# Kernel tuning notes

Hardware: AMD Instinct MI355X
Metric: run time of the kernel (lower is better)

## Reference

```python
import jax, jax.numpy as jnp
import numpy as np

B, S, D, H, F, V = 64, 64, 512, 8, 2048, 8192
L = 6
ENC_C = 2048  # InceptionV3 feature channels
NEG_INF = jnp.float32(-jnp.inf)


def _layernorm(x, g, b, eps=1e-3):
    mu = jnp.mean(x, axis=-1, keepdims=True)
    var = jnp.var(x, axis=-1, keepdims=True)
    return (x - mu) * jax.lax.rsqrt(var + eps) * g + b


def _mha(q_in, kv_in, Wq, Wk, Wv, Wo, causal=False):
    Bq, Sq, Dm = q_in.shape
    Sk = kv_in.shape[1]
    dh = Dm // H
    q = (q_in @ Wq).reshape(Bq, Sq, H, dh)
    k = (kv_in @ Wk).reshape(Bq, Sk, H, dh)
    v = (kv_in @ Wv).reshape(Bq, Sk, H, dh)
    scores = jnp.einsum('bqhd,bkhd->bhqk', q, k) / jnp.sqrt(jnp.float32(dh))
    if causal:
        mask = jnp.tril(jnp.ones((Sq, Sk), dtype=bool))
        scores = jnp.where(mask, scores, jnp.float32(-1e9))
    a = jax.nn.softmax(scores, axis=-1)
    o = jnp.einsum('bhqk,bkhd->bqhd', a, v).reshape(Bq, Sq, Dm)
    return o @ Wo


def replacement_mask(targets):
    # out[b,i,v] = -inf iff some j<=i has targets[b,j]==v and v!=0
    valid = (targets != 0)[..., None].astype(jnp.float32)  # (B,S,1)
    oh = jax.nn.one_hot(targets, V, dtype=jnp.float32) * valid  # (B,S,V)
    seen = jnp.cumsum(oh, axis=1) > 0
    return jnp.where(seen, NEG_INF, jnp.float32(0.0))


def setup_inputs() -> dict:
    key = jax.random.key(0)
    ks = jax.random.split(key, 32)
    n = lambda i, shp, sc=0.02: jax.random.normal(ks[i], shp, jnp.float32) * sc
    inp = {
        'enc_feat': jax.random.normal(ks[0], (B, 8, 8, ENC_C), jnp.float32),
        'targets': jax.random.randint(ks[1], (B, S), 0, V, jnp.int32),
        'conv_w': n(2, (ENC_C, D)), 'conv_b': jnp.zeros((D,), jnp.float32),
        'tok_emb': n(3, (V, D)), 'pos_emb': n(4, (S, D)),
        'Wq_s': n(5, (L, D, D)), 'Wk_s': n(6, (L, D, D)),
        'Wv_s': n(7, (L, D, D)), 'Wo_s': n(8, (L, D, D)),
        'Wq_c': n(9, (L, D, D)), 'Wk_c': n(10, (L, D, D)),
        'Wv_c': n(11, (L, D, D)), 'Wo_c': n(12, (L, D, D)),
        'W1': n(13, (L, D, F)), 'fb1': jnp.zeros((L, F), jnp.float32),
        'W2': n(14, (L, F, D)), 'fb2': jnp.zeros((L, D), jnp.float32),
        'g1': jnp.ones((L, D), jnp.float32), 'be1': jnp.zeros((L, D), jnp.float32),
        'g2': jnp.ones((L, D), jnp.float32), 'be2': jnp.zeros((L, D), jnp.float32),
        'g3': jnp.ones((L, D), jnp.float32), 'be3': jnp.zeros((L, D), jnp.float32),
        'Wout': n(15, (D, V)), 'bout': jnp.zeros((V,), jnp.float32),
    }
    return inp


def reference(enc_feat, conv_w, conv_b, tok_emb, pos_emb,
              Wq_s, Wk_s, Wv_s, Wo_s, Wq_c, Wk_c, Wv_c, Wo_c,
              W1, fb1, W2, fb2, g1, be1, g2, be2, g3, be3,
              Wout, bout, targets):
    # 1x1 conv == per-pixel matmul, then flatten spatial -> (B, 64, D)
    enc = enc_feat.reshape(B, -1, ENC_C) @ conv_w + conv_b
    # decoder: token + positional embedding
    x = tok_emb[targets] + pos_emb[None, :, :]
    for l in range(L):
        a1 = _mha(x, x, Wq_s[l], Wk_s[l], Wv_s[l], Wo_s[l], causal=True)
        x = _layernorm(x + a1, g1[l], be1[l])
        a2 = _mha(x, enc, Wq_c[l], Wk_c[l], Wv_c[l], Wo_c[l])
        x = _layernorm(x + a2, g2[l], be2[l])
        ff = jax.nn.relu(x @ W1[l] + fb1[l]) @ W2[l] + fb2[l]
        x = _layernorm(x + ff, g3[l], be3[l])
    logits = x @ Wout + bout
    return logits + replacement_mask(targets)
```

## Files before the change

kernel.cpp:

```cpp
#include <hip/hip_runtime.h>
#include <cstdint>
#include <cstddef>

#define SS   64
#define BB   64
#define DM   512
#define NH   8
#define DH   64
#define FF   2048
#define VV   8192
#define LL   6
#define ENCC 2048
#define MR   4096

#define MASK_SENTINEL -3.0e38f

typedef unsigned short u16;
typedef __attribute__((ext_vector_type(8))) short bf16x8;
typedef __attribute__((ext_vector_type(4))) float f32x4;

__device__ __forceinline__ u16 f2b(float f) {
    union { float f; uint32_t u; } c; c.f = f;
    uint32_t u = c.u;
    return (u16)((u + 0x7fffu + ((u >> 16) & 1u)) >> 16);
}
__device__ __forceinline__ float blo(uint32_t p) {
    union { uint32_t u; float f; } c; c.u = p << 16; return c.f;
}
__device__ __forceinline__ float bhi(uint32_t p) {
    union { uint32_t u; float f; } c; c.u = p & 0xffff0000u; return c.f;
}

#define GLL(g, l) __builtin_amdgcn_global_load_lds( \
    (const __attribute__((address_space(1))) void*)(g), \
    (__attribute__((address_space(3))) void*)(l), 16, 0, 0)

template<int BMT>
__global__ __launch_bounds__(256) void gemm_bf16(
    const u16* __restrict__ A, const u16* __restrict__ BT,
    const float* __restrict__ bias, u16* __restrict__ Cb,
    int K, int ldc, int relu, int nsplit,
    const u16* __restrict__ A2, const u16* __restrict__ BT2,
    u16* __restrict__ C2, int ldc2)
{
    constexpr int WM = BMT / 2;
    constexpr int AI = WM / 16;
    __shared__ __align__(16) char smem[16384];
    u16* As = (u16*)smem;
    u16* Bs = As + BMT * 32;
    const int tid = threadIdx.x;
    const int wave = tid >> 6, lane = tid & 63;

    int bx = blockIdx.x;
    const u16* Ab = A; const u16* Bb = BT; u16* Cp = Cb; int ld = ldc;
    const float* bi = bias; int rl = relu;
    if (bx >= nsplit) { bx -= nsplit; Ab = A2; Bb = BT2; Cp = C2; ld = ldc2; bi = nullptr; rl = 0; }

    const int m0 = blockIdx.y * BMT, n0 = bx * 128;
    const int srow = wave * 16 + (lane >> 2);
    const int scol = (lane & 3) * 8;
    const u16* Ap  = Ab + (size_t)(m0 + srow) * K + scol;
    const u16* Bp  = Bb + (size_t)(n0 + srow) * K + scol;
    const u16* Ap2 = Ap + (size_t)64 * K;
    const u16* Bp2 = Bp + (size_t)64 * K;
    u16* AsW = As + wave * 16 * 32;
    u16* BsW = Bs + wave * 16 * 32;

    const int wm = wave >> 1, wn = wave & 1;
    const int q = lane >> 4, mr = lane & 15;
    const u16* aRd = As + (size_t)(wm * WM + mr) * 32 + q * 8;
    const u16* bRd = Bs + (size_t)(wn * 64 + mr) * 32 + q * 8;

    f32x4 acc[AI][4];
    const f32x4 z = {0.f, 0.f, 0.f, 0.f};
#pragma unroll
    for (int i = 0; i < AI; i++)
#pragma unroll
        for (int j = 0; j < 4; j++) acc[i][j] = z;

    for (int k0 = 0; k0 < K; k0 += 32) {
        GLL(Ap, AsW);
        if constexpr (BMT == 128) GLL(Ap2, AsW + 64 * 32);
        GLL(Bp, BsW);
        GLL(Bp2, BsW + 64 * 32);
        Ap += 32; Ap2 += 32; Bp += 32; Bp2 += 32;
        __syncthreads();
        bf16x8 af[AI], bfr[4];
#pragma unroll
        for (int i = 0; i < AI; i++) af[i]  = *(const bf16x8*)(aRd + (size_t)i * 16 * 32);
#pragma unroll
        for (int j = 0; j < 4; j++) bfr[j] = *(const bf16x8*)(bRd + (size_t)j * 16 * 32);
#pragma unroll
        for (int i = 0; i < AI; i++)
#pragma unroll
            for (int j = 0; j < 4; j++)
                acc[i][j] = __builtin_amdgcn_mfma_f32_16x16x32_bf16(af[i], bfr[j], acc[i][j], 0, 0, 0);
        __syncthreads();
    }

    float* ep = (float*)smem + wave * 1024;
    const int lq = lane >> 4, lmr = lane & 15;
    const int colb = n0 + wn * 64 + lmr * 4;
    float4 b4 = make_float4(0.f, 0.f, 0.f, 0.f);
    if (bi) b4 = *(const float4*)(bi + colb);
#pragma unroll
    for (int i = 0; i < AI; i++) {
#pragma unroll
        for (int j = 0; j < 4; j++)
#pragma unroll
            for (int r = 0; r < 4; r++)
                ep[(q * 4 + r) * 64 + j * 16 + mr] = acc[i][j][r];
        __syncthreads();
#pragma unroll
        for (int p = 0; p < 4; p++) {
            const int lr = p * 4 + lq;
            float4 v = *(const float4*)(ep + lr * 64 + lmr * 4);
            v.x += b4.x; v.y += b4.y; v.z += b4.z; v.w += b4.w;
            if (rl) {
                v.x = fmaxf(v.x, 0.f); v.y = fmaxf(v.y, 0.f);
                v.z = fmaxf(v.z, 0.f); v.w = fmaxf(v.w, 0.f);
            }
            uint2 pk;
            pk.x = (uint32_t)f2b(v.x) | ((uint32_t)f2b(v.y) << 16);
            pk.y = (uint32_t)f2b(v.z) | ((uint32_t)f2b(v.w) << 16);
            const int row = m0 + wm * WM + i * 16 + lr;
            *(uint2*)(Cp + (size_t)row * ld + colb) = pk;
        }
        __syncthreads();
    }
}

__global__ __launch_bounds__(256) void gemm_logits_mfma(
    const u16* __restrict__ A, const u16* __restrict__ BT,
    const float* __restrict__ bias, const int* __restrict__ fo,
    float* __restrict__ C, int K)
{
    __shared__ __align__(16) char smem[16384];
    u16* As = (u16*)smem;
    u16* Bs = As + 128 * 32;
    const int tid = threadIdx.x;
    const int wave = tid >> 6, lane = tid & 63;
    const int m0 = blockIdx.y * 128, n0 = blockIdx.x * 128;

    const int srow = wave * 16 + (lane >> 2);
    const int scol = (lane & 3) * 8;
    const u16* Ap  = A  + (size_t)(m0 + srow) * K + scol;
    const u16* Bp  = BT + (size_t)(n0 + srow) * K + scol;
    const u16* Ap2 = Ap + (size_t)64 * K;
    const u16* Bp2 = Bp + (size_t)64 * K;
    u16* AsW = As + wave * 16 * 32;
    u16* BsW = Bs + wave * 16 * 32;

    const int wm = wave >> 1, wn = wave & 1;
    const int q = lane >> 4, mr = lane & 15;
    const u16* aRd = As + (size_t)(wm * 64 + mr) * 32 + q * 8;
    const u16* bRd = Bs + (size_t)(wn * 64 + mr) * 32 + q * 8;

    f32x4 acc[4][4];
    const f32x4 z = {0.f, 0.f, 0.f, 0.f};
#pragma unroll
    for (int i = 0; i < 4; i++)
#pragma unroll
        for (int j = 0; j < 4; j++) acc[i][j] = z;

    for (int k0 = 0; k0 < K; k0 += 32) {
        GLL(Ap,  AsW);
        GLL(Ap2, AsW + 64 * 32);
        GLL(Bp,  BsW);
        GLL(Bp2, BsW + 64 * 32);
        Ap += 32; Ap2 += 32; Bp += 32; Bp2 += 32;
        __syncthreads();
        bf16x8 af[4], bfr[4];
#pragma unroll
        for (int i = 0; i < 4; i++) af[i]  = *(const bf16x8*)(aRd + (size_t)i * 16 * 32);
#pragma unroll
        for (int j = 0; j < 4; j++) bfr[j] = *(const bf16x8*)(bRd + (size_t)j * 16 * 32);
#pragma unroll
        for (int i = 0; i < 4; i++)
#pragma unroll
            for (int j = 0; j < 4; j++)
                acc[i][j] = __builtin_amdgcn_mfma_f32_16x16x32_bf16(af[i], bfr[j], acc[i][j], 0, 0, 0);
        __syncthreads();
    }

    float* ep = (float*)smem + wave * 1024;
    const int lq = lane >> 4, lmr = lane & 15;
    const int colb = n0 + wn * 64 + lmr * 4;
    const float4 b4 = *(const float4*)(bias + colb);
#pragma unroll
    for (int i = 0; i < 4; i++) {
#pragma unroll
        for (int j = 0; j < 4; j++)
#pragma unroll
            for (int r = 0; r < 4; r++)
                ep[(q * 4 + r) * 64 + j * 16 + mr] = acc[i][j][r];
        __syncthreads();
#pragma unroll
        for (int p = 0; p < 4; p++) {
            const int lr = p * 4 + lq;
            const int row = m0 + wm * 64 + i * 16 + lr;
            const int b = row >> 6, pos = row & 63;
            float4 v = *(const float4*)(ep + lr * 64 + lmr * 4);
            const int4 f4 = *(const int4*)(fo + (size_t)b * VV + colb);
            v.x = (f4.x <= pos) ? MASK_SENTINEL : v.x + b4.x;
            v.y = (f4.y <= pos) ? MASK_SENTINEL : v.y + b4.y;
            v.z = (f4.z <= pos) ? MASK_SENTINEL : v.z + b4.z;
            v.w = (f4.w <= pos) ? MASK_SENTINEL : v.w + b4.w;
            *(float4*)(C + (size_t)row * VV + colb) = v;
        }
        __syncthreads();
    }
}

struct TPB {
    const float* s[8];
    u16* d[8];
    long dz[8];
};

__global__ __launch_bounds__(256) void transpose8_kernel(TPB t)
{
    __shared__ float tl[32][33];
    const int zz = blockIdx.z;
    const int m = zz / 6, l = zz - m * 6;
    const float* in = t.s[m] + (size_t)l * 262144;
    u16* out = t.d[m] + (size_t)l * t.dz[m];
    const int r0 = blockIdx.y * 32, c0 = blockIdx.x * 32;
    const int tx = threadIdx.x & 31, ty = threadIdx.x >> 5;
#pragma unroll
    for (int i = 0; i < 4; i++)
        tl[ty + 8 * i][tx] = in[(size_t)(r0 + ty + 8 * i) * 512 + c0 + tx];
    __syncthreads();
#pragma unroll
    for (int i = 0; i < 4; i++)
        out[(size_t)(c0 + ty + 8 * i) * 512 + r0 + tx] = f2b(tl[tx][ty + 8 * i]);
}

__global__ __launch_bounds__(256) void transpose_bf16_kernel(
    const float* __restrict__ in, u16* __restrict__ out,
    int R, int C, size_t in_z, size_t out_z)
{
    __shared__ float tl[32][33];
    in  += (size_t)blockIdx.z * in_z;
    out += (size_t)blockIdx.z * out_z;
    const int r0 = blockIdx.y * 32, c0 = blockIdx.x * 32;
    const int tx = threadIdx.x & 31, ty = threadIdx.x >> 5;
#pragma unroll
    for (int i = 0; i < 4; i++)
        tl[ty + 8 * i][tx] = in[(size_t)(r0 + ty + 8 * i) * C + c0 + tx];
    __syncthreads();
#pragma unroll
    for (int i = 0; i < 4; i++)
        out[(size_t)(c0 + ty + 8 * i) * R + r0 + tx] = f2b(tl[tx][ty + 8 * i]);
}

__global__ __launch_bounds__(256) void convert_bf16_kernel(
    const float* __restrict__ in, u16* __restrict__ out)
{
    const int idx = blockIdx.x * 256 + threadIdx.x;
    float4 v = *reinterpret_cast<const float4*>(in + (size_t)idx * 4);
    uint2 p;
    p.x = (uint32_t)f2b(v.x) | ((uint32_t)f2b(v.y) << 16);
    p.y = (uint32_t)f2b(v.z) | ((uint32_t)f2b(v.w) << 16);
    *reinterpret_cast<uint2*>(out + (size_t)idx * 4) = p;
}

__global__ __launch_bounds__(256) void attn_kernel(
    const u16* __restrict__ qg, int qld,
    const u16* __restrict__ kg, const u16* __restrict__ vg, int kvld,
    u16* __restrict__ og, int causal)
{
    __shared__ float qs[SS][68];
    __shared__ float ks[SS][68];
    __shared__ float vs[SS][68];
    __shared__ float red[SS][8];
    float (*ps)[68] = qs;

    const int tid = threadIdx.x;
    const int bh = blockIdx.x;
    const int b = bh >> 3, h = bh & 7;
    const size_t qbase = (size_t)b * SS * qld + (size_t)h * DH;
    const size_t kbase = (size_t)b * SS * kvld + (size_t)h * DH;
    const size_t obase = (size_t)b * SS * DM + (size_t)h * DH;

#pragma unroll
    for (int it = 0; it < 4; it++) {
        int idx = tid + 256 * it;
        int s = idx >> 4;
        int d4 = (idx & 15) << 2;
        uint2 a = *(const uint2*)(qg + qbase + (size_t)s * qld + d4);
        qs[s][d4 + 0] = blo(a.x); qs[s][d4 + 1] = bhi(a.x);
        qs[s][d4 + 2] = blo(a.y); qs[s][d4 + 3] = bhi(a.y);
        uint2 c = *(const uint2*)(kg + kbase + (size_t)s * kvld + d4);
        ks[s][d4 + 0] = blo(c.x); ks[s][d4 + 1] = bhi(c.x);
        ks[s][d4 + 2] = blo(c.y); ks[s][d4 + 3] = bhi(c.y);
        uint2 e = *(const uint2*)(vg + kbase + (size_t)s * kvld + d4);
        vs[s][d4 + 0] = blo(e.x); vs[s][d4 + 1] = bhi(e.x);
        vs[s][d4 + 2] = blo(e.y); vs[s][d4 + 3] = bhi(e.y);
    }
    __syncthreads();

    const int r = tid >> 2, c = tid & 3;

    float sc[16];
#pragma unroll
    for (int jj = 0; jj < 16; jj++) sc[jj] = 0.f;
    for (int d4 = 0; d4 < 64; d4 += 4) {
        float4 qv = *reinterpret_cast<const float4*>(&qs[r][d4]);
#pragma unroll
        for (int jj = 0; jj < 16; jj++) {
            int j = jj * 4 + c;
            float4 kv = *reinterpret_cast<const float4*>(&ks[j][d4]);
            sc[jj] += qv.x * kv.x + qv.y * kv.y + qv.z * kv.z + qv.w * kv.w;
        }
    }
    float mx = -1e30f;
#pragma unroll
    for (int jj = 0; jj < 16; jj++) {
        int j = jj * 4 + c;
        float s_ = sc[jj] * 0.125f;
        if (causal && j > r) s_ = -1e9f;
        sc[jj] = s_;
        mx = fmaxf(mx, s_);
    }
    red[r][c] = mx;
    __syncthreads();
    float m = fmaxf(fmaxf(red[r][0], red[r][1]), fmaxf(red[r][2], red[r][3]));
    float sum = 0.f;
#pragma unroll
    for (int jj = 0; jj < 16; jj++) {
        float p = expf(sc[jj] - m);
        sc[jj] = p;
        sum += p;
    }
    red[r][4 + c] = sum;
    __syncthreads();
    float tot = red[r][4] + red[r][5] + red[r][6] + red[r][7];
    float inv = 1.f / tot;
#pragma unroll
    for (int jj = 0; jj < 16; jj++) ps[r][jj * 4 + c] = sc[jj] * inv;
    __syncthreads();

    float acc[16];
#pragma unroll
    for (int i = 0; i < 16; i++) acc[i] = 0.f;
    for (int j = 0; j < 64; j++) {
        float pj = ps[r][j];
#pragma unroll
        for (int dd = 0; dd < 4; dd++) {
            float4 vv = *reinterpret_cast<const float4*>(&vs[j][c * 16 + dd * 4]);
            acc[dd * 4 + 0] += pj * vv.x;
            acc[dd * 4 + 1] += pj * vv.y;
            acc[dd * 4 + 2] += pj * vv.z;
            acc[dd * 4 + 3] += pj * vv.w;
        }
    }
#pragma unroll
    for (int dd = 0; dd < 4; dd++) {
        uint2 p;
        p.x = (uint32_t)f2b(acc[dd * 4 + 0]) | ((uint32_t)f2b(acc[dd * 4 + 1]) << 16);
        p.y = (uint32_t)f2b(acc[dd * 4 + 2]) | ((uint32_t)f2b(acc[dd * 4 + 3]) << 16);
        *reinterpret_cast<uint2*>(&og[obase + (size_t)r * DM + c * 16 + dd * 4]) = p;
    }
}

__global__ __launch_bounds__(256) void add_ln_kernel(
    const float* __restrict__ x, const u16* __restrict__ a,
    const float* __restrict__ g, const float* __restrict__ be,
    float* __restrict__ y, u16* __restrict__ yb)
{
    const int wave = threadIdx.x >> 6, lane = threadIdx.x & 63;
    const int row = blockIdx.x * 4 + wave;
    const float* xr = x + (size_t)row * DM;
    const u16* ar = a + (size_t)row * DM;
    float* yr = y + (size_t)row * DM;
    u16* ybr = yb + (size_t)row * DM;

    float vbuf[8];
    float sum = 0.f, sq = 0.f;
#pragma unroll
    for (int i = 0; i < 2; i++) {
        int d = lane * 8 + i * 4;
        float4 xv = *reinterpret_cast<const float4*>(&xr[d]);
        uint2 av = *(const uint2*)(ar + d);
        float a0 = blo(av.x), a1 = bhi(av.x), a2 = blo(av.y), a3 = bhi(av.y);
        float v0 = xv.x + a0, v1 = xv.y + a1, v2 = xv.z + a2, v3 = xv.w + a3;
        vbuf[i * 4 + 0] = v0; vbuf[i * 4 + 1] = v1;
        vbuf[i * 4 + 2] = v2; vbuf[i * 4 + 3] = v3;
        sum += v0 + v1 + v2 + v3;
        sq += v0 * v0 + v1 * v1 + v2 * v2 + v3 * v3;
    }
#pragma unroll
    for (int off = 32; off; off >>= 1) {
        sum += __shfl_xor(sum, off, 64);
        sq  += __shfl_xor(sq, off, 64);
    }
    float mean = sum * (1.f / 512.f);
    float var = sq * (1.f / 512.f) - mean * mean;
    float rs = rsqrtf(var + 1e-3f);
#pragma unroll
    for (int i = 0; i < 2; i++) {
        int d = lane * 8 + i * 4;
        float4 gv = *reinterpret_cast<const float4*>(&g[d]);
        float4 bv = *reinterpret_cast<const float4*>(&be[d]);
        float4 ov;
        ov.x = (vbuf[i * 4 + 0] - mean) * rs * gv.x + bv.x;
        ov.y = (vbuf[i * 4 + 1] - mean) * rs * gv.y + bv.y;
        ov.z = (vbuf[i * 4 + 2] - mean) * rs * gv.z + bv.z;
        ov.w = (vbuf[i * 4 + 3] - mean) * rs * gv.w + bv.w;
        *reinterpret_cast<float4*>(&yr[d]) = ov;
        uint2 p;
        p.x = (uint32_t)f2b(ov.x) | ((uint32_t)f2b(ov.y) << 16);
        p.y = (uint32_t)f2b(ov.z) | ((uint32_t)f2b(ov.w) << 16);
        *reinterpret_cast<uint2*>(&ybr[d]) = p;
    }
}

__global__ __launch_bounds__(256) void embed_kernel(
    const int* __restrict__ targets, const float* __restrict__ tok,
    const float* __restrict__ pos, float* __restrict__ x, u16* __restrict__ xb)
{
    int idx = blockIdx.x * 256 + threadIdx.x;
    int row = idx >> 7;
    int d4 = (idx & 127) << 2;
    int s = row & 63;
    int t = targets[row];
    float4 tv = *reinterpret_cast<const float4*>(&tok[(size_t)t * DM + d4]);
    float4 pv = *reinterpret_cast<const float4*>(&pos[(size_t)s * DM + d4]);
    float4 ov = make_float4(tv.x + pv.x, tv.y + pv.y, tv.z + pv.z, tv.w + pv.w);
    *reinterpret_cast<float4*>(&x[(size_t)row * DM + d4]) = ov;
    uint2 p;
    p.x = (uint32_t)f2b(ov.x) | ((uint32_t)f2b(ov.y) << 16);
    p.y = (uint32_t)f2b(ov.z) | ((uint32_t)f2b(ov.w) << 16);
    *reinterpret_cast<uint2*>(&xb[(size_t)row * DM + d4]) = p;
}

__global__ __launch_bounds__(256) void init_fo_kernel(int* __restrict__ fo)
{
    fo[blockIdx.x * 256 + threadIdx.x] = SS;
}

__global__ __launch_bounds__(256) void scatter_fo_kernel(
    const int* __restrict__ targets, int* __restrict__ fo)
{
    int i = blockIdx.x * 256 + threadIdx.x;
    int t = targets[i];
    if (t != 0) atomicMin(&fo[(size_t)(i >> 6) * VV + t], i & 63);
}

extern "C" void kernel_launch(void* const* d_in, const int* in_sizes, int n_in,
                              void* d_out, int out_size, void* d_ws, size_t ws_size,
                              hipStream_t stream)
{
    const float* enc_feat = (const float*)d_in[0];
    const int*   targets  = (const int*)d_in[1];
    const float* conv_w   = (const float*)d_in[2];
    const float* conv_b   = (const float*)d_in[3];
    const float* tok_emb  = (const float*)d_in[4];
    const float* pos_emb  = (const float*)d_in[5];
    const float* Wq_s     = (const float*)d_in[6];
    const float* Wk_s     = (const float*)d_in[7];
    const float* Wv_s     = (const float*)d_in[8];
    const float* Wo_s     = (const float*)d_in[9];
    const float* Wq_c     = (const float*)d_in[10];
    const float* Wk_c     = (const float*)d_in[11];
    const float* Wv_c     = (const float*)d_in[12];
    const float* Wo_c     = (const float*)d_in[13];
    const float* W1       = (const float*)d_in[14];
    const float* fb1      = (const float*)d_in[15];
    const float* W2       = (const float*)d_in[16];
    const float* fb2      = (const float*)d_in[17];
    const float* g1       = (const float*)d_in[18];
    const float* be1      = (const float*)d_in[19];
    const float* g2       = (const float*)d_in[20];
    const float* be2      = (const float*)d_in[21];
    const float* g3       = (const float*)d_in[22];
    const float* be3      = (const float*)d_in[23];
    const float* Wout     = (const float*)d_in[24];
    const float* bout     = (const float*)d_in[25];
    float* out = (float*)d_out;

    u16* base = (u16*)d_ws;
    float* x   = (float*)d_ws;
    u16* xb    = base + 4194304;
    u16* projb = base + 6291456;
    u16* qcb   = base + 8388608;
    u16* attnb = base + 10485760;
    u16* encb  = base + 12582912;
    u16* big   = base + 14680064;
    int* fo    = (int*)(base + 23068672);
    u16* qkvT  = base + 24117248;
    u16* woTs  = base + 28835840;
    u16* wqTc  = base + 30408704;
    u16* kvTc  = base + 31981568;
    u16* woTc  = base + 35127296;
    u16* w1T   = base + 36700160;
    u16* w2T   = base + 42991616;
    u16* cvT   = base + 49283072;
    u16* woutT = base + 50331648;

    const dim3 blk(256);

    init_fo_kernel<<<dim3(BB * VV / 256), blk, 0, stream>>>(fo);
    scatter_fo_kernel<<<dim3(MR / 256), blk, 0, stream>>>(targets, fo);
    embed_kernel<<<dim3(MR * DM / 4 / 256), blk, 0, stream>>>(targets, tok_emb, pos_emb, x, xb);
    convert_bf16_kernel<<<dim3(MR * ENCC / 4 / 256), blk, 0, stream>>>(enc_feat, big);

    TPB tp;
    tp.s[0] = Wq_s; tp.d[0] = qkvT;          tp.dz[0] = 786432;
    tp.s[1] = Wk_s; tp.d[1] = qkvT + 262144; tp.dz[1] = 786432;
    tp.s[2] = Wv_s; tp.d[2] = qkvT + 524288; tp.dz[2] = 786432;
    tp.s[3] = Wo_s; tp.d[3] = woTs;          tp.dz[3] = 262144;
    tp.s[4] = Wq_c; tp.d[4] = wqTc;          tp.dz[4] = 262144;
    tp.s[5] = Wk_c; tp.d[5] = kvTc;          tp.dz[5] = 524288;
    tp.s[6] = Wv_c; tp.d[6] = kvTc + 262144; tp.dz[6] = 524288;
    tp.s[7] = Wo_c; tp.d[7] = woTc;          tp.dz[7] = 262144;
    transpose8_kernel<<<dim3(16, 16, 48), blk, 0, stream>>>(tp);
    transpose_bf16_kernel<<<dim3(64, 16, 6), blk, 0, stream>>>(W1, w1T, 512, 2048, 1048576, 1048576);
    transpose_bf16_kernel<<<dim3(16, 64, 6), blk, 0, stream>>>(W2, w2T, 2048, 512, 1048576, 1048576);
    transpose_bf16_kernel<<<dim3(16, 64, 1), blk, 0, stream>>>(conv_w, cvT, 2048, 512, 0, 0);
    transpose_bf16_kernel<<<dim3(256, 16, 1), blk, 0, stream>>>(Wout, woutT, 512, 8192, 0, 0);

    gemm_bf16<64><<<dim3(4, 64), blk, 0, stream>>>(big, cvT, conv_b, encb, ENCC, DM, 0, 9999,
                                                   nullptr, nullptr, nullptr, 0);

    for (int l = 0; l < LL; l++) {
        gemm_bf16<128><<<dim3(12, 32), blk, 0, stream>>>(xb, qkvT + (size_t)l * 786432, nullptr,
                                                         big, DM, 1536, 0, 9999,
                                                         nullptr, nullptr, nullptr, 0);
        attn_kernel<<<dim3(BB * NH), blk, 0, stream>>>(big, 1536, big + 512, big + 1024, 1536, attnb, 1);
        gemm_bf16<64><<<dim3(4, 64), blk, 0, stream>>>(attnb, woTs + (size_t)l * 262144, nullptr,
                                                       projb, DM, DM, 0, 9999,
                                                       nullptr, nullptr, nullptr, 0);
        add_ln_kernel<<<dim3(MR / 4), blk, 0, stream>>>(x, projb, g1 + l * DM, be1 + l * DM, x, xb);
        gemm_bf16<128><<<dim3(12, 32), blk, 0, stream>>>(xb, wqTc + (size_t)l * 262144, nullptr,
                                                         qcb, DM, DM, 0, 4,
                                                         encb, kvTc + (size_t)l * 524288, big, 1024);
        attn_kernel<<<dim3(BB * NH), blk, 0, stream>>>(qcb, 512, big, big + 512, 1024, attnb, 0);
        gemm_bf16<64><<<dim3(4, 64), blk, 0, stream>>>(attnb, woTc + (size_t)l * 262144, nullptr,
                                                       projb, DM, DM, 0, 9999,
                                                       nullptr, nullptr, nullptr, 0);
        add_ln_kernel<<<dim3(MR / 4), blk, 0, stream>>>(x, projb, g2 + l * DM, be2 + l * DM, x, xb);
        gemm_bf16<128><<<dim3(16, 32), blk, 0, stream>>>(xb, w1T + (size_t)l * 1048576,
                                                         fb1 + (size_t)l * FF, big, DM, FF, 1, 9999,
                                                         nullptr, nullptr, nullptr, 0);
        gemm_bf16<64><<<dim3(4, 64), blk, 0, stream>>>(big, w2T + (size_t)l * 1048576,
                                                       fb2 + (size_t)l * DM, projb, FF, DM, 0, 9999,
                                                       nullptr, nullptr, nullptr, 0);
        add_ln_kernel<<<dim3(MR / 4), blk, 0, stream>>>(x, projb, g3 + l * DM, be3 + l * DM, x, xb);
    }

    gemm_logits_mfma<<<dim3(64, 32), blk, 0, stream>>>(xb, woutT, bout, fo, out, DM);
}
```

Before: 1.444 ms.

## Double-buffer GEMM LDS tiles and hoist cross-attention K/V projections out of layer loop

The GEMM kernels now use two LDS buffers, issuing the global-to-LDS loads for the next K-slice before computing on the current one and dropping one barrier per iteration. Separately, the cross-attention K/V projections of the encoder output for all six layers are computed in one large GEMM before the layer loop, since they depend only on the encoder. The per-layer cross-attention launch then only projects Q, using the smaller tile config. Doubling LDS use may lower occupancy, and the batched K/V buffer needs extra workspace.

```diff
diff --git a/kernel.cpp b/kernel.cpp
--- a/kernel.cpp
+++ b/kernel.cpp
@@ -45,9 +45,8 @@
 {
     constexpr int WM = BMT / 2;
     constexpr int AI = WM / 16;
-    __shared__ __align__(16) char smem[16384];
-    u16* As = (u16*)smem;
-    u16* Bs = As + BMT * 32;
+    constexpr int TILE = (BMT + 128) * 32;
+    __shared__ __align__(16) u16 smem[2 * TILE];
     const int tid = threadIdx.x;
     const int wave = tid >> 6, lane = tid & 63;
 
@@ -63,13 +62,13 @@
     const u16* Bp  = Bb + (size_t)(n0 + srow) * K + scol;
     const u16* Ap2 = Ap + (size_t)64 * K;
     const u16* Bp2 = Bp + (size_t)64 * K;
-    u16* AsW = As + wave * 16 * 32;
-    u16* BsW = Bs + wave * 16 * 32;
+    const int aW = wave * 16 * 32;
+    const int bW = BMT * 32 + wave * 16 * 32;
 
     const int wm = wave >> 1, wn = wave & 1;
     const int q = lane >> 4, mr = lane & 15;
-    const u16* aRd = As + (size_t)(wm * WM + mr) * 32 + q * 8;
-    const u16* bRd = Bs + (size_t)(wn * 64 + mr) * 32 + q * 8;
+    const int aRd = (wm * WM + mr) * 32 + q * 8;
+    const int bRd = BMT * 32 + (wn * 64 + mr) * 32 + q * 8;
 
     f32x4 acc[AI][4];
     const f32x4 z = {0.f, 0.f, 0.f, 0.f};
@@ -78,24 +77,36 @@
 #pragma unroll
         for (int j = 0; j < 4; j++) acc[i][j] = z;
 
+    GLL(Ap, smem + aW);
+    if constexpr (BMT == 128) GLL(Ap2, smem + aW + 64 * 32);
+    GLL(Bp, smem + bW);
+    GLL(Bp2, smem + bW + 64 * 32);
+    Ap += 32; Ap2 += 32; Bp += 32; Bp2 += 32;
+    __syncthreads();
+
+    int cur = 0;
     for (int k0 = 0; k0 < K; k0 += 32) {
-        GLL(Ap, AsW);
-        if constexpr (BMT == 128) GLL(Ap2, AsW + 64 * 32);
-        GLL(Bp, BsW);
-        GLL(Bp2, BsW + 64 * 32);
-        Ap += 32; Ap2 += 32; Bp += 32; Bp2 += 32;
-        __syncthreads();
+        if (k0 + 32 < K) {
+            u16* nb = smem + (cur ^ 1) * TILE;
+            GLL(Ap, nb + aW);
+            if constexpr (BMT == 128) GLL(Ap2, nb + aW + 64 * 32);
+            GLL(Bp, nb + bW);
+            GLL(Bp2, nb + bW + 64 * 32);
+            Ap += 32; Ap2 += 32; Bp += 32; Bp2 += 32;
+        }
+        const u16* cb = smem + cur * TILE;
         bf16x8 af[AI], bfr[4];
 #pragma unroll
-        for (int i = 0; i < AI; i++) af[i]  = *(const bf16x8*)(aRd + (size_t)i * 16 * 32);
-#pragma unroll
-        for (int j = 0; j < 4; j++) bfr[j] = *(const bf16x8*)(bRd + (size_t)j * 16 * 32);
+        for (int i = 0; i < AI; i++) af[i]  = *(const bf16x8*)(cb + aRd + (size_t)i * 16 * 32);
+#pragma unroll
+        for (int j = 0; j < 4; j++) bfr[j] = *(const bf16x8*)(cb + bRd + (size_t)j * 16 * 32);
 #pragma unroll
         for (int i = 0; i < AI; i++)
 #pragma unroll
             for (int j = 0; j < 4; j++)
                 acc[i][j] = __builtin_amdgcn_mfma_f32_16x16x32_bf16(af[i], bfr[j], acc[i][j], 0, 0, 0);
         __syncthreads();
+        cur ^= 1;
     }
 
     float* ep = (float*)smem + wave * 1024;
@@ -135,9 +146,8 @@
     const float* __restrict__ bias, const int* __restrict__ fo,
     float* __restrict__ C, int K)
 {
-    __shared__ __align__(16) char smem[16384];
-    u16* As = (u16*)smem;
-    u16* Bs = As + 128 * 32;
+    constexpr int TILE = 256 * 32;
+    __shared__ __align__(16) u16 smem[2 * TILE];
     const int tid = threadIdx.x;
     const int wave = tid >> 6, lane = tid & 63;
     const int m0 = blockIdx.y * 128, n0 = blockIdx.x * 128;
@@ -148,13 +158,13 @@
     const u16* Bp  = BT + (size_t)(n0 + srow) * K + scol;
     const u16* Ap2 = Ap + (size_t)64 * K;
     const u16* Bp2 = Bp + (size_t)64 * K;
-    u16* AsW = As + wave * 16 * 32;
-    u16* BsW = Bs + wave * 16 * 32;
+    const int aW = wave * 16 * 32;
+    const int bW = 128 * 32 + wave * 16 * 32;
 
     const int wm = wave >> 1, wn = wave & 1;
     const int q = lane >> 4, mr = lane & 15;
-    const u16* aRd = As + (size_t)(wm * 64 + mr) * 32 + q * 8;
-    const u16* bRd = Bs + (size_t)(wn * 64 + mr) * 32 + q * 8;
+    const int aRd = (wm * 64 + mr) * 32 + q * 8;
+    const int bRd = 128 * 32 + (wn * 64 + mr) * 32 + q * 8;
 
     f32x4 acc[4][4];
     const f32x4 z = {0.f, 0.f, 0.f, 0.f};
@@ -163,24 +173,36 @@
 #pragma unroll
         for (int j = 0; j < 4; j++) acc[i][j] = z;
 
+    GLL(Ap,  smem + aW);
+    GLL(Ap2, smem + aW + 64 * 32);
+    GLL(Bp,  smem + bW);
+    GLL(Bp2, smem + bW + 64 * 32);
+    Ap += 32; Ap2 += 32; Bp += 32; Bp2 += 32;
+    __syncthreads();
+
+    int cur = 0;
     for (int k0 = 0; k0 < K; k0 += 32) {
-        GLL(Ap,  AsW);
-        GLL(Ap2, AsW + 64 * 32);
-        GLL(Bp,  BsW);
-        GLL(Bp2, BsW + 64 * 32);
-        Ap += 32; Ap2 += 32; Bp += 32; Bp2 += 32;
-        __syncthreads();
+        if (k0 + 32 < K) {
+            u16* nb = smem + (cur ^ 1) * TILE;
+            GLL(Ap,  nb + aW);
+            GLL(Ap2, nb + aW + 64 * 32);
+            GLL(Bp,  nb + bW);
+            GLL(Bp2, nb + bW + 64 * 32);
+            Ap += 32; Ap2 += 32; Bp += 32; Bp2 += 32;
+        }
+        const u16* cb = smem + cur * TILE;
         bf16x8 af[4], bfr[4];
 #pragma unroll
-        for (int i = 0; i < 4; i++) af[i]  = *(const bf16x8*)(aRd + (size_t)i * 16 * 32);
-#pragma unroll
-        for (int j = 0; j < 4; j++) bfr[j] = *(const bf16x8*)(bRd + (size_t)j * 16 * 32);
+        for (int i = 0; i < 4; i++) af[i]  = *(const bf16x8*)(cb + aRd + (size_t)i * 16 * 32);
+#pragma unroll
+        for (int j = 0; j < 4; j++) bfr[j] = *(const bf16x8*)(cb + bRd + (size_t)j * 16 * 32);
 #pragma unroll
         for (int i = 0; i < 4; i++)
 #pragma unroll
             for (int j = 0; j < 4; j++)
                 acc[i][j] = __builtin_amdgcn_mfma_f32_16x16x32_bf16(af[i], bfr[j], acc[i][j], 0, 0, 0);
         __syncthreads();
+        cur ^= 1;
     }
 
     float* ep = (float*)smem + wave * 1024;
@@ -498,6 +520,7 @@
     u16* w2T   = base + 42991616;
     u16* cvT   = base + 49283072;
     u16* woutT = base + 50331648;
+    u16* kvAll = base + 54525952;
 
     const dim3 blk(256);
 
@@ -524,6 +547,9 @@
     gemm_bf16<64><<<dim3(4, 64), blk, 0, stream>>>(big, cvT, conv_b, encb, ENCC, DM, 0, 9999,
                                                    nullptr, nullptr, nullptr, 0);
 
+    gemm_bf16<128><<<dim3(48, 32), blk, 0, stream>>>(encb, kvTc, nullptr, kvAll, DM, 6144, 0, 9999,
+                                                     nullptr, nullptr, nullptr, 0);
+
     for (int l = 0; l < LL; l++) {
         gemm_bf16<128><<<dim3(12, 32), blk, 0, stream>>>(xb, qkvT + (size_t)l * 786432, nullptr,
                                                          big, DM, 1536, 0, 9999,
@@ -533,10 +559,12 @@
                                                        projb, DM, DM, 0, 9999,
                                                        nullptr, nullptr, nullptr, 0);
         add_ln_kernel<<<dim3(MR / 4), blk, 0, stream>>>(x, projb, g1 + l * DM, be1 + l * DM, x, xb);
-        gemm_bf16<128><<<dim3(12, 32), blk, 0, stream>>>(xb, wqTc + (size_t)l * 262144, nullptr,
-                                                         qcb, DM, DM, 0, 4,
-                                                         encb, kvTc + (size_t)l * 524288, big, 1024);
-        attn_kernel<<<dim3(BB * NH), blk, 0, stream>>>(qcb, 512, big, big + 512, 1024, attnb, 0);
+        gemm_bf16<64><<<dim3(4, 64), blk, 0, stream>>>(xb, wqTc + (size_t)l * 262144, nullptr,
+                                                       qcb, DM, DM, 0, 9999,
+                                                       nullptr, nullptr, nullptr, 0);
+        attn_kernel<<<dim3(BB * NH), blk, 0, stream>>>(qcb, 512,
+                                                       kvAll + (size_t)l * 1024,
+                                                       kvAll + (size_t)l * 1024 + 512, 6144, attnb, 0);
         gemm_bf16<64><<<dim3(4, 64), blk, 0, stream>>>(attnb, woTc + (size_t)l * 262144, nullptr,
                                                        projb, DM, DM, 0, 9999,
                                                        nullptr, nullptr, nullptr, 0);
```

Measured after the change: 1.331 ms. -7.8%, faster.
